# Kernel tuning notes

Measured on AMD Instinct MI355X. Metric: run time of the kernel, lower is better.

## Reference

```python
import jax, jax.numpy as jnp
import numpy as np

NPOINT = 1024
BRANCHES = [(0.4, 32), (0.8, 64)]  # (radius, nsample)
SPECS = [[67, 64, 64, 128], [67, 64, 128, 256]]  # mlp specs after use_xyz (+3)
EPS = 1e-5


def setup_inputs() -> dict:
    key = jax.random.key(0)
    ks = jax.random.split(key, 16)
    B, N, C = 8, 8192, 64
    inp = {
        "xyz": jax.random.normal(ks[0], (B, N, 3), jnp.float32),
        "features": jax.random.normal(ks[1], (B, C, N), jnp.float32),
    }
    ki = 2
    for bi, spec in enumerate(SPECS):
        for li in range(3):
            o, i = spec[li + 1], spec[li]
            inp[f"w{bi}_{li}"] = jax.random.normal(ks[ki], (o, i), jnp.float32) * (1.0 / np.sqrt(i)); ki += 1
            inp[f"g{bi}_{li}"] = jnp.ones((o,), jnp.float32)
            inp[f"b{bi}_{li}"] = jnp.zeros((o,), jnp.float32)
    return inp


def fps(pts, npoint):
    # pts: [B, N+1, 3] (mean point prepended); sequential farthest point sampling
    B, N1, _ = pts.shape

    def step(carry, _):
        dist, far = carry
        idx3 = jnp.broadcast_to(far[:, None, None], (B, 1, 3))
        centroid = jnp.take_along_axis(pts, idx3, axis=1)  # [B,1,3]
        d = jnp.sum((pts - centroid) ** 2, axis=-1)        # [B,N+1]
        dist = jnp.minimum(dist, d)
        far2 = jnp.argmax(dist, axis=-1)
        return (dist, far2), centroid[:, 0, :]

    dist0 = jnp.full((B, N1), 1e10, jnp.float32)
    far0 = jnp.zeros((B,), jnp.int32)
    _, locs = jax.lax.scan(step, (dist0, far0), None, length=npoint)
    return jnp.transpose(locs, (1, 0, 2))  # [B, npoint, 3]


def ball_query(xyz, new_xyz, radius, nsample):
    # first <=nsample indices with dist^2 < radius^2, padded with first valid (0 if none)
    B, N, _ = xyz.shape
    d2 = jnp.sum((new_xyz[:, :, None, :] - xyz[:, None, :, :]) ** 2, axis=-1)  # [B,S,N]
    score = jnp.where(d2 < radius * radius, jnp.arange(N, dtype=jnp.int32), N)
    vals, _ = jax.lax.top_k(-score, nsample)  # smallest scores = earliest valid indices
    idx = -vals                               # [B,S,nsample], N marks invalid
    first = idx[..., :1]
    first = jnp.where(first < N, first, 0)
    return jnp.where(idx < N, idx, first)


def _forward(xyz, features, params):
    mean = jnp.mean(xyz, axis=1, keepdims=True)
    pts = jnp.concatenate([mean, xyz], axis=1)          # prepend mean point
    new_xyz = jax.lax.stop_gradient(fps(pts, NPOINT))   # [B,npoint,3] (torch no_grad)
    outs = []
    for (radius, nsample), layers in zip(BRANCHES, params):
        idx = ball_query(xyz, new_xyz, radius, nsample)           # [B,S,K]
        gxyz = jax.vmap(lambda p, i: p[i])(xyz, idx)              # [B,S,K,3]
        rel = jnp.transpose(gxyz - new_xyz[:, :, None, :], (0, 3, 1, 2))  # [B,3,S,K]
        gfeat = jax.vmap(lambda f, i: f[:, i])(features, idx)     # [B,C,S,K]
        x = jnp.concatenate([rel, gfeat], axis=1)                 # [B,3+C,S,K]
        for W, g, b in layers:  # Conv2d 1x1 (no bias) + BatchNorm (train stats) + ReLU
            x = jnp.einsum('oi,bisk->bosk', W, x)
            m = jnp.mean(x, axis=(0, 2, 3), keepdims=True)
            v = jnp.var(x, axis=(0, 2, 3), keepdims=True)
            x = (x - m) / jnp.sqrt(v + EPS) * g[None, :, None, None] + b[None, :, None, None]
            x = jax.nn.relu(x)
        outs.append(jnp.max(x, axis=3))                           # [B,Cout,S]
    return new_xyz, jnp.concatenate(outs, axis=1)


def reference(xyz, features,
              w0_0, g0_0, b0_0, w0_1, g0_1, b0_1, w0_2, g0_2, b0_2,
              w1_0, g1_0, b1_0, w1_1, g1_1, b1_1, w1_2, g1_2, b1_2):
    params = [
        [(w0_0, g0_0, b0_0), (w0_1, g0_1, b0_1), (w0_2, g0_2, b0_2)],
        [(w1_0, g1_0, b1_0), (w1_1, g1_1, b1_1), (w1_2, g1_2, b1_2)],
    ]
    return _forward(xyz, features, params)
```

## Files before the change

### kernel.cpp

```cpp
#include <hip/hip_runtime.h>
#include <hip/hip_bf16.h>
#include <cstdint>


typedef __attribute__((ext_vector_type(8))) short short8;
typedef __attribute__((ext_vector_type(4))) float f32x4;
typedef __attribute__((ext_vector_type(2))) float f32x2;

__device__ __forceinline__ float bf2f(unsigned short u) {
    return __uint_as_float(((unsigned)u) << 16);
}
__device__ __forceinline__ unsigned short f2bf(float f) {
    unsigned u = __float_as_uint(f);
    return (unsigned short)((u + 0x7fffu + ((u >> 16) & 1u)) >> 16);
}

__device__ __forceinline__ float wave_red_max_f32(float v) {
#define DPPSTEP(ctrl)                                                                  \
    {                                                                                  \
        int _t = __builtin_amdgcn_update_dpp((int)0xFF800000, __float_as_int(v), ctrl, \
                                             0xf, 0xf, false);                         \
        v = fmaxf(v, __int_as_float(_t));                                              \
    }
    DPPSTEP(0x111) DPPSTEP(0x112) DPPSTEP(0x114) DPPSTEP(0x118) DPPSTEP(0x142) DPPSTEP(0x143)
#undef DPPSTEP
    return v;
}
__device__ __forceinline__ unsigned wave_red_min_u32(unsigned v) {
#define DPPSTEP(ctrl)                                                                   \
    {                                                                                   \
        unsigned _t = (unsigned)__builtin_amdgcn_update_dpp((int)0xFFFFFFFF, (int)v,    \
                                                            ctrl, 0xf, 0xf, false);     \
        v = v < _t ? v : _t;                                                            \
    }
    DPPSTEP(0x111) DPPSTEP(0x112) DPPSTEP(0x114) DPPSTEP(0x118) DPPSTEP(0x142) DPPSTEP(0x143)
#undef DPPSTEP
    return v;
}
__device__ __forceinline__ unsigned long long u64max(unsigned long long a, unsigned long long b) {
    return a > b ? a : b;
}
__device__ __forceinline__ unsigned u32min(unsigned a, unsigned b) { return a < b ? a : b; }

static const size_t OFF_WBF   = 0;
static const size_t OFF_STATS = 262144;
static const size_t STATS_BYTES = 720896;
static const size_t OFF_AFF   = 1048576;
static const size_t OFF_IDX0  = 2097152;
static const size_t OFF_IDX1  = 3145728;
static const size_t OFF_MX    = 5242880;
static const size_t OFF_MN    = 13631488;
static const size_t OFF_Y0    = 22020096;
static const size_t OFF_Y1    = 90177536;
static const size_t OFF_FEATT = 211812352;

__global__ __launch_bounds__(256) void fused_pre(
    const float* __restrict__ xyz, const float* __restrict__ feat,
    float* __restrict__ newxyz, unsigned short* __restrict__ ft,
    const float* __restrict__ w0, const float* __restrict__ w1, const float* __restrict__ w2,
    const float* __restrict__ w3, const float* __restrict__ w4, const float* __restrict__ w5,
    unsigned short* __restrict__ wb) {
    __shared__ union alignas(16) SM {
        struct {
            float ptsx[8200], ptsy[8200], ptsz[8200];
            float ldsM[16][3];
            float meanv[3];
            unsigned long long sKey[2][4];
            float cbuf[3072];
        } f;
        float tile[64][65];
    } sm;
    const int tid = threadIdx.x;

    if (blockIdx.x >= 1032) {
        int id = (int)(blockIdx.x - 1032) * 256 + tid;
        const int psz[6] = {6144, 4096, 8192, 6144, 8192, 32768};
        const int Kp[6] = {96, 64, 64, 96, 64, 128};
        const int Ks[6] = {67, 64, 64, 67, 64, 128};
        const float* wp[6] = {w0, w1, w2, w3, w4, w5};
        int off = 0;
        for (int l = 0; l < 6; ++l) {
            if (id < off + psz[l]) {
                int e = id - off;
                int m = e / Kp[l], k = e - m * Kp[l];
                float v = (k < Ks[l]) ? wp[l][m * Ks[l] + k] : 0.f;
                wb[id] = f2bf(v);
                return;
            }
            off += psz[l];
        }
        return;
    }

    if (blockIdx.x >= 8) {
        int tb = (int)blockIdx.x - 8;
        int b = tb >> 7;
        int j0 = (tb & 127) * 64;
#pragma unroll
        for (int i = 0; i < 16; ++i) {
            int e = i * 256 + tid;
            int c = e >> 6, j = e & 63;
            sm.tile[j][c] = feat[((size_t)b * 64 + c) * 8192 + j0 + j];
        }
        __syncthreads();
#pragma unroll
        for (int i = 0; i < 16; ++i) {
            int e = i * 256 + tid;
            int j = e >> 6, c = e & 63;
            ft[((size_t)(b * 8192 + j0 + j)) * 96 + 3 + c] = f2bf(sm.tile[j][c]);
        }
        if (tid < 64) {
            int j = tid;
            size_t base = ((size_t)(b * 8192 + j0 + j)) * 96;
            const float* xp = xyz + ((size_t)b * 8192 + j0 + j) * 3;
            ft[base + 0] = f2bf(xp[0]);
            ft[base + 1] = f2bf(xp[1]);
            ft[base + 2] = f2bf(xp[2]);
        } else if (tid < 128) {
            int j = tid - 64;
            size_t base = ((size_t)(b * 8192 + j0 + j)) * 96;
            for (int c = 67; c < 96; ++c) ft[base + c] = 0;
        }
        return;
    }

    const int b = blockIdx.x;
    const int t = tid;
    const int lane = t & 63, wv = t >> 6;
    const float* xb = xyz + (size_t)b * 8192 * 3;

    f32x2 px[16], py[16], pz[16], d[16];
#pragma unroll
    for (int k = 0; k < 16; ++k) {
        int q0 = t + 256 * (2 * k);
        int q1 = t + 256 * (2 * k + 1);
        px[k].x = xb[q0 * 3 + 0]; px[k].y = xb[q1 * 3 + 0];
        py[k].x = xb[q0 * 3 + 1]; py[k].y = xb[q1 * 3 + 1];
        pz[k].x = xb[q0 * 3 + 2]; pz[k].y = xb[q1 * 3 + 2];
        d[k].x = 1e10f; d[k].y = 1e10f;
        sm.f.ptsx[q0 + 1] = px[k].x; sm.f.ptsx[q1 + 1] = px[k].y;
        sm.f.ptsy[q0 + 1] = py[k].x; sm.f.ptsy[q1 + 1] = py[k].y;
        sm.f.ptsz[q0 + 1] = pz[k].x; sm.f.ptsz[q1 + 1] = pz[k].y;
    }
    {
        float sx[4], sy[4], sz[4];
#pragma unroll
        for (int m = 0; m < 4; ++m) {
            int u = (t + 256 * m + 1023) & 1023;
            float ax = 0.f, ay = 0.f, az = 0.f;
#pragma unroll
            for (int jj = 0; jj < 8; ++jj) {
                int ia = u + 1024 * jj;
                ax += xb[ia * 3 + 0]; ay += xb[ia * 3 + 1]; az += xb[ia * 3 + 2];
            }
            sx[m] = ax; sy[m] = ay; sz[m] = az;
        }
#pragma unroll
        for (int off = 32; off; off >>= 1) {
#pragma unroll
            for (int m = 0; m < 4; ++m) {
                sx[m] += __shfl_xor(sx[m], off, 64);
                sy[m] += __shfl_xor(sy[m], off, 64);
                sz[m] += __shfl_xor(sz[m], off, 64);
            }
        }
        if (lane == 0) {
#pragma unroll
            for (int m = 0; m < 4; ++m) {
                sm.f.ldsM[wv + 4 * m][0] = sx[m];
                sm.f.ldsM[wv + 4 * m][1] = sy[m];
                sm.f.ldsM[wv + 4 * m][2] = sz[m];
            }
        }
    }
    __syncthreads();
    if (t < 3) {
        float s = 0.f;
        for (int w = 0; w < 16; ++w) s += sm.f.ldsM[w][t];
        sm.f.meanv[t] = s * (1.f / 8192.f);
    }
    __syncthreads();
    float cx = sm.f.meanv[0], cy = sm.f.meanv[1], cz = sm.f.meanv[2];
    const float mmx = cx, mmy = cy, mmz = cz;
    float dm = 1e10f;
    if (t == 0) { sm.f.ptsx[0] = cx; sm.f.ptsy[0] = cy; sm.f.ptsz[0] = cz; }
    __syncthreads();

    for (int it = 0; it < 1024; ++it) {
        if (t == 0) {
            sm.f.cbuf[it * 3 + 0] = cx;
            sm.f.cbuf[it * 3 + 1] = cy;
            sm.f.cbuf[it * 3 + 2] = cz;
        }
        f32x2 c0, c1, c2, vm2;
        c0.x = cx; c0.y = cx; c1.x = cy; c1.y = cy; c2.x = cz; c2.y = cz;
        vm2.x = -1e30f; vm2.y = -1e30f;
        {
#pragma clang fp contract(off)
#pragma unroll
            for (int k = 0; k < 16; ++k) {
                f32x2 dx = px[k] - c0;
                f32x2 dy = py[k] - c1;
                f32x2 dz = pz[k] - c2;
                f32x2 dd = (dx * dx + dy * dy) + dz * dz;
                f32x2 nd = __builtin_elementwise_min(d[k], dd);
                d[k] = nd;
                vm2 = __builtin_elementwise_max(vm2, nd);
            }
        }
        float vmax = fmaxf(vm2.x, vm2.y);
        if (t == 0) {
            float dx = __fsub_rn(mmx, cx);
            float dy = __fsub_rn(mmy, cy);
            float dz = __fsub_rn(mmz, cz);
            float dd = __fadd_rn(__fadd_rn(__fmul_rn(dx, dx), __fmul_rn(dy, dy)), __fmul_rn(dz, dz));
            dm = fminf(dm, dd);
            vmax = fmaxf(vmax, dm);
        }
        float wm = wave_red_max_f32(vmax);
        float bmaxw = __int_as_float(__builtin_amdgcn_readlane(__float_as_int(wm), 63));
        unsigned m2[16];
#pragma unroll
        for (int k = 0; k < 16; ++k) {
            unsigned i0 = (d[k].x == bmaxw) ? (unsigned)(t + 256 * (2 * k) + 1) : 0xFFFFFFFFu;
            unsigned i1 = (d[k].y == bmaxw) ? (unsigned)(t + 256 * (2 * k + 1) + 1) : 0xFFFFFFFFu;
            m2[k] = u32min(i0, i1);
        }
#pragma unroll
        for (int s = 8; s; s >>= 1)
#pragma unroll
            for (int k = 0; k < s; ++k) m2[k] = u32min(m2[k], m2[k + s]);
        unsigned mi = m2[0];
        if (t == 0 && dm == bmaxw) mi = 0u;
        unsigned wmin = wave_red_min_u32(mi);
        unsigned miw = (unsigned)__builtin_amdgcn_readlane((int)wmin, 63);
        int par = it & 1;
        if (lane == 0)
            sm.f.sKey[par][wv] = ((unsigned long long)__float_as_uint(bmaxw) << 32) |
                                 (unsigned long long)(8192u - miw);
        __syncthreads();
        unsigned long long ka[4];
#pragma unroll
        for (int i = 0; i < 4; ++i) ka[i] = sm.f.sKey[par][i];
        unsigned long long kk = u64max(u64max(ka[0], ka[1]), u64max(ka[2], ka[3]));
        int far = 8192 - (int)(unsigned)(kk & 0xffffffffull);
        cx = sm.f.ptsx[far];
        cy = sm.f.ptsy[far];
        cz = sm.f.ptsz[far];
    }
    __syncthreads();
    float* ob = newxyz + (size_t)b * 3072;
#pragma unroll
    for (int i = 0; i < 12; ++i) ob[t + 256 * i] = sm.f.cbuf[t + 256 * i];
}

__global__ void ball_query2(const float* __restrict__ xyz, const float* __restrict__ newxyz,
                            int* __restrict__ idx0, int* __restrict__ idx1) {
    int bid = blockIdx.x;
    int br = (bid >= 2048);
    int K = br ? 64 : 32;
    float r2 = br ? (0.8f * 0.8f) : (0.4f * 0.4f);
    int* idxout = br ? idx1 : idx0;
    int wid = (((bid & 2047) * 256) + threadIdx.x) >> 6;
    int lane = threadIdx.x & 63;
    int b = wid >> 10;
    const float* q = newxyz + (size_t)wid * 3;
    float qx = q[0], qy = q[1], qz = q[2];
    const float* xb = xyz + (size_t)b * 8192 * 3;
    int* out = idxout + (size_t)wid * K;
    int count = 0;
    int first = 0;
    for (int base = 0; base < 8192 && count < K; base += 64) {
        int j = base + lane;
        float dx = __fsub_rn(xb[j * 3 + 0], qx);
        float dy = __fsub_rn(xb[j * 3 + 1], qy);
        float dz = __fsub_rn(xb[j * 3 + 2], qz);
        float d2 = __fadd_rn(__fadd_rn(__fmul_rn(dx, dx), __fmul_rn(dy, dy)), __fmul_rn(dz, dz));
        bool in = d2 < r2;
        unsigned long long m = __ballot(in);
        if (count == 0 && m) first = base + __ffsll((long long)m) - 1;
        if (in) {
            int pos = count + __popcll(m & ((1ull << lane) - 1ull));
            if (pos < K) out[pos] = j;
        }
        count += __popcll(m);
    }
    if (count < K) {
        int fillv = (count > 0) ? first : 0;
        for (int p = count + lane; p < K; p += 64) out[p] = fillv;
    }
}

template <int Mp, int Kp, int IN_MODE, int OUT_MODE, int KSH, int NT>
__global__ __launch_bounds__(256) void gemm_mfma(
    const unsigned short* __restrict__ Wb, const unsigned short* __restrict__ Xin,
    const float* __restrict__ aff, const int* __restrict__ idx,
    const unsigned short* __restrict__ ftp, const float* __restrict__ newxyz,
    unsigned short* __restrict__ Yout, float* __restrict__ MX, float* __restrict__ MN,
    float* __restrict__ statS, float* __restrict__ statQ) {
    constexpr int MT = Mp / 64;
    constexpr int KS = Kp / 32;
    constexpr int NC = NT * 16;
    constexpr int NCHUNK = NT * KS * 64;
    __shared__ unsigned short Bs[NCHUNK * 8];
    __shared__ float sAux[NT * 64];
    int* sAuxI = (int*)sAux;

    const int tid = threadIdx.x;
    const int w = tid >> 6;
    const int lane = tid & 63;
    const int n = lane & 15;
    const int quad = lane >> 4;
    const int rbase = w * (Mp / 4);
    const long col0 = (long)blockIdx.x * NC;

    short8 a[MT][KS];
#pragma unroll
    for (int mt = 0; mt < MT; ++mt)
#pragma unroll
        for (int ks = 0; ks < KS; ++ks)
            a[mt][ks] = *(const short8*)(Wb + (size_t)(rbase + mt * 16 + n) * Kp + ks * 32 + quad * 8);

    if constexpr (IN_MODE == 0) {
        for (int c = tid; c < NC; c += 256) {
            long colg = col0 + c;
            sAuxI[c] = idx[colg];
            long sk = colg >> KSH;
            sAux[NC + c] = newxyz[sk * 3 + 0];
            sAux[2 * NC + c] = newxyz[sk * 3 + 1];
            sAux[3 * NC + c] = newxyz[sk * 3 + 2];
        }
    } else {
        if (tid < 2 * Kp) sAux[tid] = aff[tid];
    }
    __syncthreads();

#pragma unroll
    for (int i = 0; i < NCHUNK / 256; ++i) {
        int p = i * 256 + tid;
        int pl = p & 63;
        int pn = pl & 15;
        int pq = pl >> 4;
        int rest = p >> 6;
        int pks = rest % KS;
        int pnt = rest / KS;
        int col = pnt * 16 + pn;
        int kc = pks * 4 + pq;
        short8 v;
        if constexpr (IN_MODE == 0) {
            const int bb = (int)(col0 >> (KSH + 10));
            int j = sAuxI[col];
            v = *(const short8*)(ftp + ((long)(bb * 8192 + j)) * 96 + kc * 8);
            if (kc == 0) {
                v[0] = (short)f2bf(bf2f((unsigned short)v[0]) - sAux[NC + col]);
                v[1] = (short)f2bf(bf2f((unsigned short)v[1]) - sAux[2 * NC + col]);
                v[2] = (short)f2bf(bf2f((unsigned short)v[2]) - sAux[3 * NC + col]);
            }
        } else {
            short8 raw = *(const short8*)(Xin + (col0 + col) * (long)Kp + kc * 8);
#pragma unroll
            for (int e = 0; e < 8; ++e) {
                float xf = bf2f((unsigned short)raw[e]);
                xf = fmaxf(fmaf(xf, sAux[kc * 8 + e], sAux[Kp + kc * 8 + e]), 0.f);
                v[e] = (short)f2bf(xf);
            }
        }
        *(short8*)(&Bs[p * 8]) = v;
    }
    __syncthreads();

    f32x4 acc[MT][NT];
#pragma unroll
    for (int mt = 0; mt < MT; ++mt)
#pragma unroll
        for (int nt = 0; nt < NT; ++nt)
#pragma unroll
            for (int r = 0; r < 4; ++r) acc[mt][nt][r] = 0.f;

#pragma unroll
    for (int ks = 0; ks < KS; ++ks) {
#pragma unroll
        for (int nt = 0; nt < NT; ++nt) {
            short8 bfr = *(const short8*)(&Bs[((nt * KS + ks) * 64 + lane) * 8]);
#pragma unroll
            for (int mt = 0; mt < MT; ++mt)
                acc[mt][nt] = __builtin_amdgcn_mfma_f32_16x16x32_bf16(a[mt][ks], bfr, acc[mt][nt], 0, 0, 0);
        }
    }

    const int slot = (int)(blockIdx.x & 127);
#pragma unroll
    for (int mt = 0; mt < MT; ++mt)
#pragma unroll
        for (int r = 0; r < 4; ++r) {
            float s = 0.f, q = 0.f;
#pragma unroll
            for (int nt = 0; nt < NT; ++nt) {
                float v = acc[mt][nt][r];
                s += v;
                q = fmaf(v, v, q);
            }
#pragma unroll
            for (int off = 1; off < 16; off <<= 1) {
                s += __shfl_xor(s, off, 16);
                q += __shfl_xor(q, off, 16);
            }
            if (n == 0) {
                int ch = rbase + mt * 16 + quad * 4 + r;
                atomicAdd(statS + (size_t)ch * 128 + slot, s);
                atomicAdd(statQ + (size_t)ch * 128 + slot, q);
            }
        }

    if constexpr (OUT_MODE == 0) {
#pragma unroll
        for (int mt = 0; mt < MT; ++mt)
#pragma unroll
            for (int nt = 0; nt < NT; ++nt) {
                long col = col0 + nt * 16 + n;
                unsigned p0 = f2bf(acc[mt][nt][0]) | ((unsigned)f2bf(acc[mt][nt][1]) << 16);
                unsigned p1 = f2bf(acc[mt][nt][2]) | ((unsigned)f2bf(acc[mt][nt][3]) << 16);
                uint2 st; st.x = p0; st.y = p1;
                *(uint2*)(Yout + col * Mp + rbase + mt * 16 + quad * 4) = st;
            }
    } else {
        constexpr int GRP = (1 << KSH) / 16;
        constexpr int NG = NT / GRP;
#pragma unroll
        for (int mt = 0; mt < MT; ++mt)
#pragma unroll
            for (int r = 0; r < 4; ++r) {
#pragma unroll
                for (int gh = 0; gh < NG; ++gh) {
                    float mx = acc[mt][GRP * gh][r], mn = acc[mt][GRP * gh][r];
#pragma unroll
                    for (int e = 1; e < GRP; ++e) {
                        mx = fmaxf(mx, acc[mt][GRP * gh + e][r]);
                        mn = fminf(mn, acc[mt][GRP * gh + e][r]);
                    }
#pragma unroll
                    for (int off = 1; off < 16; off <<= 1) {
                        mx = fmaxf(mx, __shfl_xor(mx, off, 16));
                        mn = fminf(mn, __shfl_xor(mn, off, 16));
                    }
                    if (n == 0) {
                        int ch = rbase + mt * 16 + quad * 4 + r;
                        long g = (col0 >> KSH) + gh;
                        MX[(long)ch * 8192 + g] = mx;
                        MN[(long)ch * 8192 + g] = mn;
                    }
                }
            }
    }
}

__global__ void finalize_kernel(const float* __restrict__ sS, const float* __restrict__ sQ,
                                const float* __restrict__ g, const float* __restrict__ b,
                                float* __restrict__ aff, int C, float invCount) {
    int c = threadIdx.x + blockIdx.x * blockDim.x;
    if (c >= C) return;
    float s = 0.f, q = 0.f;
    for (int k = 0; k < 128; ++k) { s += sS[c * 128 + k]; q += sQ[c * 128 + k]; }
    float mean = s * invCount;
    float var = fmaxf(q * invCount - mean * mean, 0.f);
    float sc = g[c] / sqrtf(var + 1e-5f);
    float sh = b[c] - mean * sc;
    aff[c] = sc;
    aff[C + c] = sh;
}

__global__ void final_out_kernel(const float* __restrict__ MX, const float* __restrict__ MN,
                                 const float* __restrict__ aff, float* __restrict__ out1,
                                 int Cout, int cOff) {
    long i = (long)blockIdx.x * 256 + threadIdx.x;
    int c = (int)(i >> 13);
    int gidx = (int)(i & 8191);
    int b = gidx >> 10, s = gidx & 1023;
    float sc = aff[c], sh = aff[Cout + c];
    float v = fmaxf(fmaxf(sc * MX[i] + sh, sc * MN[i] + sh), 0.f);
    out1[((long)b * 384 + cOff + c) * 1024 + s] = v;
}

extern "C" void kernel_launch(void* const* d_in, const int* in_sizes, int n_in,
                              void* d_out, int out_size, void* d_ws, size_t ws_size,
                              hipStream_t stream) {
    const float* xyz = (const float*)d_in[0];
    const float* feat = (const float*)d_in[1];
    const float *W[6], *G[6], *Bi[6];
    for (int l = 0; l < 6; ++l) {
        W[l] = (const float*)d_in[2 + l * 3];
        G[l] = (const float*)d_in[3 + l * 3];
        Bi[l] = (const float*)d_in[4 + l * 3];
    }
    char* ws = (char*)d_ws;
    float* out0 = (float*)d_out;
    float* out1 = (float*)d_out + 24576;

    unsigned short* wb = (unsigned short*)(ws + OFF_WBF);
    float* stats = (float*)(ws + OFF_STATS);
    float* affine = (float*)(ws + OFF_AFF);
    int* idx0 = (int*)(ws + OFF_IDX0);
    int* idx1 = (int*)(ws + OFF_IDX1);
    float* mx = (float*)(ws + OFF_MX);
    float* mn = (float*)(ws + OFF_MN);
    unsigned short* y0 = (unsigned short*)(ws + OFF_Y0);
    unsigned short* y1 = (unsigned short*)(ws + OFF_Y1);
    unsigned short* ftp = (unsigned short*)(ws + OFF_FEATT);

    hipMemsetAsync(stats, 0, STATS_BYTES, stream);
    fused_pre<<<1288, 256, 0, stream>>>(xyz, feat, out0, ftp, W[0], W[1], W[2], W[3], W[4],
                                        W[5], wb);
    ball_query2<<<4096, 256, 0, stream>>>(xyz, out0, idx0, idx1);

    const int wOff[6] = {0, 6144, 10240, 18432, 24576, 32768};
    int stOff[6], afOff[6];
    {
        const int Cs[6] = {64, 64, 128, 64, 128, 256};
        int so = 0, ao = 0;
        for (int l = 0; l < 6; ++l) {
            stOff[l] = so; so += Cs[l] * 256;
            afOff[l] = ao; ao += Cs[l] * 2;
        }
    }

    for (int br = 0; br < 2; ++br) {
        const int K = br ? 64 : 32;
        const long NCOL = 8L * 1024 * K;
        int* idx = br ? idx1 : idx0;
        const int l0 = br * 3, l1 = br * 3 + 1, l2 = br * 3 + 2;
        const int M2 = br ? 256 : 128;
        const float invCount = 1.f / (float)NCOL;
        const int nblk256 = (int)(NCOL / 256);
        const int nblk128 = (int)(NCOL / 128);
        const int nblk64 = (int)(NCOL / 64);

        if (br == 0) {
            gemm_mfma<64, 96, 0, 0, 5, 16><<<nblk256, 256, 0, stream>>>(
                wb + wOff[l0], nullptr, nullptr, idx, ftp, out0, y0, nullptr, nullptr,
                stats + stOff[l0], stats + stOff[l0] + 64 * 128);
            finalize_kernel<<<1, 256, 0, stream>>>(stats + stOff[l0], stats + stOff[l0] + 64 * 128,
                                                   G[l0], Bi[l0], affine + afOff[l0], 64, invCount);
            gemm_mfma<64, 64, 1, 0, 5, 16><<<nblk256, 256, 0, stream>>>(
                wb + wOff[l1], y0, affine + afOff[l0], nullptr, nullptr, nullptr, y1, nullptr,
                nullptr, stats + stOff[l1], stats + stOff[l1] + 64 * 128);
            finalize_kernel<<<1, 256, 0, stream>>>(stats + stOff[l1], stats + stOff[l1] + 64 * 128,
                                                   G[l1], Bi[l1], affine + afOff[l1], 64, invCount);
            gemm_mfma<128, 64, 1, 1, 5, 8><<<nblk128, 256, 0, stream>>>(
                wb + wOff[l2], y1, affine + afOff[l1], nullptr, nullptr, nullptr, nullptr, mx, mn,
                stats + stOff[l2], stats + stOff[l2] + 128 * 128);
            finalize_kernel<<<1, 256, 0, stream>>>(stats + stOff[l2], stats + stOff[l2] + 128 * 128,
                                                   G[l2], Bi[l2], affine + afOff[l2], 128, invCount);
        } else {
            gemm_mfma<64, 96, 0, 0, 6, 16><<<nblk256, 256, 0, stream>>>(
                wb + wOff[l0], nullptr, nullptr, idx, ftp, out0, y0, nullptr, nullptr,
                stats + stOff[l0], stats + stOff[l0] + 64 * 128);
            finalize_kernel<<<1, 256, 0, stream>>>(stats + stOff[l0], stats + stOff[l0] + 64 * 128,
                                                   G[l0], Bi[l0], affine + afOff[l0], 64, invCount);
            gemm_mfma<128, 64, 1, 0, 6, 8><<<nblk128, 256, 0, stream>>>(
                wb + wOff[l1], y0, affine + afOff[l0], nullptr, nullptr, nullptr, y1, nullptr,
                nullptr, stats + stOff[l1], stats + stOff[l1] + 128 * 128);
            finalize_kernel<<<1, 256, 0, stream>>>(stats + stOff[l1], stats + stOff[l1] + 128 * 128,
                                                   G[l1], Bi[l1], affine + afOff[l1], 128, invCount);
            gemm_mfma<256, 128, 1, 1, 6, 4><<<nblk64, 256, 0, stream>>>(
                wb + wOff[l2], y1, affine + afOff[l1], nullptr, nullptr, nullptr, nullptr, mx, mn,
                stats + stOff[l2], stats + stOff[l2] + 256 * 128);
            finalize_kernel<<<1, 256, 0, stream>>>(stats + stOff[l2], stats + stOff[l2] + 256 * 128,
                                                   G[l2], Bi[l2], affine + afOff[l2], 256, invCount);
        }

        final_out_kernel<<<(M2 * 8192) / 256, 256, 0, stream>>>(mx, mn, affine + afOff[l2], out1,
                                                                M2, br ? 128 : 0);
    }
}
```

Baseline: 1.635 ms.

## Add persistent double-buffered GEMM for MLP layers and single-pass FPS argmax

The FPS loop now tracks the running max value and its index in one pass, replacing the second equality scan and min-reduction tree over all distances, and reads the per-wave keys with vector loads. The later MLP GEMMs become persistent kernels with a fixed grid of 768 blocks. Each block double-buffers the next tile's normalised and activated input in shared memory while computing the current tile, and keeps BN statistics in registers before a final atomic flush. The gather-based first layer is split into its own kernel, and the second layer of branch 0 uses a narrower NT tile. The aim is to cut FPS per-iteration work and hide load latency in the GEMMs, at the cost of more register pressure and strided tile scheduling.

```diff
diff --git a/kernel.cpp b/kernel.cpp
--- a/kernel.cpp
+++ b/kernel.cpp
@@ -65,7 +65,7 @@
             float ptsx[8200], ptsy[8200], ptsz[8200];
             float ldsM[16][3];
             float meanv[3];
-            unsigned long long sKey[2][4];
+            alignas(16) unsigned long long sKey[2][4];
             float cbuf[3072];
         } f;
         float tile[64][65];
@@ -192,9 +192,10 @@
             sm.f.cbuf[it * 3 + 1] = cy;
             sm.f.cbuf[it * 3 + 2] = cz;
         }
-        f32x2 c0, c1, c2, vm2;
+        f32x2 c0, c1, c2;
         c0.x = cx; c0.y = cx; c1.x = cy; c1.y = cy; c2.x = cz; c2.y = cz;
-        vm2.x = -1e30f; vm2.y = -1e30f;
+        float bv = -1e30f;
+        unsigned bi = 0u;
         {
 #pragma clang fp contract(off)
 #pragma unroll
@@ -205,32 +206,25 @@
                 f32x2 dd = (dx * dx + dy * dy) + dz * dz;
                 f32x2 nd = __builtin_elementwise_min(d[k], dd);
                 d[k] = nd;
-                vm2 = __builtin_elementwise_max(vm2, nd);
-            }
-        }
-        float vmax = fmaxf(vm2.x, vm2.y);
+                bool g0 = nd.x > bv;
+                bv = fmaxf(bv, nd.x);
+                bi = g0 ? (unsigned)(t + 256 * (2 * k) + 1) : bi;
+                bool g1 = nd.y > bv;
+                bv = fmaxf(bv, nd.y);
+                bi = g1 ? (unsigned)(t + 256 * (2 * k + 1) + 1) : bi;
+            }
+        }
         if (t == 0) {
             float dx = __fsub_rn(mmx, cx);
             float dy = __fsub_rn(mmy, cy);
             float dz = __fsub_rn(mmz, cz);
             float dd = __fadd_rn(__fadd_rn(__fmul_rn(dx, dx), __fmul_rn(dy, dy)), __fmul_rn(dz, dz));
             dm = fminf(dm, dd);
-            vmax = fmaxf(vmax, dm);
-        }
-        float wm = wave_red_max_f32(vmax);
+            bv = fmaxf(bv, dm);
+        }
+        float wm = wave_red_max_f32(bv);
         float bmaxw = __int_as_float(__builtin_amdgcn_readlane(__float_as_int(wm), 63));
-        unsigned m2[16];
-#pragma unroll
-        for (int k = 0; k < 16; ++k) {
-            unsigned i0 = (d[k].x == bmaxw) ? (unsigned)(t + 256 * (2 * k) + 1) : 0xFFFFFFFFu;
-            unsigned i1 = (d[k].y == bmaxw) ? (unsigned)(t + 256 * (2 * k + 1) + 1) : 0xFFFFFFFFu;
-            m2[k] = u32min(i0, i1);
-        }
-#pragma unroll
-        for (int s = 8; s; s >>= 1)
-#pragma unroll
-            for (int k = 0; k < s; ++k) m2[k] = u32min(m2[k], m2[k + s]);
-        unsigned mi = m2[0];
+        unsigned mi = (bv == bmaxw) ? bi : 0xFFFFFFFFu;
         if (t == 0 && dm == bmaxw) mi = 0u;
         unsigned wmin = wave_red_min_u32(mi);
         unsigned miw = (unsigned)__builtin_amdgcn_readlane((int)wmin, 63);
@@ -239,10 +233,9 @@
             sm.f.sKey[par][wv] = ((unsigned long long)__float_as_uint(bmaxw) << 32) |
                                  (unsigned long long)(8192u - miw);
         __syncthreads();
-        unsigned long long ka[4];
-#pragma unroll
-        for (int i = 0; i < 4; ++i) ka[i] = sm.f.sKey[par][i];
-        unsigned long long kk = u64max(u64max(ka[0], ka[1]), u64max(ka[2], ka[3]));
+        ulonglong2 kp0 = *(const ulonglong2*)&sm.f.sKey[par][0];
+        ulonglong2 kp1 = *(const ulonglong2*)&sm.f.sKey[par][2];
+        unsigned long long kk = u64max(u64max(kp0.x, kp0.y), u64max(kp1.x, kp1.y));
         int far = 8192 - (int)(unsigned)(kk & 0xffffffffull);
         cx = sm.f.ptsx[far];
         cy = sm.f.ptsy[far];
@@ -291,13 +284,11 @@
     }
 }
 
-template <int Mp, int Kp, int IN_MODE, int OUT_MODE, int KSH, int NT>
-__global__ __launch_bounds__(256) void gemm_mfma(
-    const unsigned short* __restrict__ Wb, const unsigned short* __restrict__ Xin,
-    const float* __restrict__ aff, const int* __restrict__ idx,
+template <int Mp, int Kp, int KSH, int NT>
+__global__ __launch_bounds__(256) void gemm_gather(
+    const unsigned short* __restrict__ Wb, const int* __restrict__ idx,
     const unsigned short* __restrict__ ftp, const float* __restrict__ newxyz,
-    unsigned short* __restrict__ Yout, float* __restrict__ MX, float* __restrict__ MN,
-    float* __restrict__ statS, float* __restrict__ statQ) {
+    unsigned short* __restrict__ Yout, float* __restrict__ statS, float* __restrict__ statQ) {
     constexpr int MT = Mp / 64;
     constexpr int KS = Kp / 32;
     constexpr int NC = NT * 16;
@@ -321,17 +312,13 @@
         for (int ks = 0; ks < KS; ++ks)
             a[mt][ks] = *(const short8*)(Wb + (size_t)(rbase + mt * 16 + n) * Kp + ks * 32 + quad * 8);
 
-    if constexpr (IN_MODE == 0) {
-        for (int c = tid; c < NC; c += 256) {
-            long colg = col0 + c;
-            sAuxI[c] = idx[colg];
-            long sk = colg >> KSH;
-            sAux[NC + c] = newxyz[sk * 3 + 0];
-            sAux[2 * NC + c] = newxyz[sk * 3 + 1];
-            sAux[3 * NC + c] = newxyz[sk * 3 + 2];
-        }
-    } else {
-        if (tid < 2 * Kp) sAux[tid] = aff[tid];
+    for (int c = tid; c < NC; c += 256) {
+        long colg = col0 + c;
+        sAuxI[c] = idx[colg];
+        long sk = colg >> KSH;
+        sAux[NC + c] = newxyz[sk * 3 + 0];
+        sAux[2 * NC + c] = newxyz[sk * 3 + 1];
+        sAux[3 * NC + c] = newxyz[sk * 3 + 2];
     }
     __syncthreads();
 
@@ -346,24 +333,13 @@
         int pnt = rest / KS;
         int col = pnt * 16 + pn;
         int kc = pks * 4 + pq;
-        short8 v;
-        if constexpr (IN_MODE == 0) {
-            const int bb = (int)(col0 >> (KSH + 10));
-            int j = sAuxI[col];
-            v = *(const short8*)(ftp + ((long)(bb * 8192 + j)) * 96 + kc * 8);
-            if (kc == 0) {
-                v[0] = (short)f2bf(bf2f((unsigned short)v[0]) - sAux[NC + col]);
-                v[1] = (short)f2bf(bf2f((unsigned short)v[1]) - sAux[2 * NC + col]);
-                v[2] = (short)f2bf(bf2f((unsigned short)v[2]) - sAux[3 * NC + col]);
-            }
-        } else {
-            short8 raw = *(const short8*)(Xin + (col0 + col) * (long)Kp + kc * 8);
-#pragma unroll
-            for (int e = 0; e < 8; ++e) {
-                float xf = bf2f((unsigned short)raw[e]);
-                xf = fmaxf(fmaf(xf, sAux[kc * 8 + e], sAux[Kp + kc * 8 + e]), 0.f);
-                v[e] = (short)f2bf(xf);
-            }
+        const int bb = (int)(col0 >> (KSH + 10));
+        int j = sAuxI[col];
+        short8 v = *(const short8*)(ftp + ((long)(bb * 8192 + j)) * 96 + kc * 8);
+        if (kc == 0) {
+            v[0] = (short)f2bf(bf2f((unsigned short)v[0]) - sAux[NC + col]);
+            v[1] = (short)f2bf(bf2f((unsigned short)v[1]) - sAux[2 * NC + col]);
+            v[2] = (short)f2bf(bf2f((unsigned short)v[2]) - sAux[3 * NC + col]);
         }
         *(short8*)(&Bs[p * 8]) = v;
     }
@@ -412,46 +388,191 @@
             }
         }
 
-    if constexpr (OUT_MODE == 0) {
+#pragma unroll
+    for (int mt = 0; mt < MT; ++mt)
+#pragma unroll
+        for (int nt = 0; nt < NT; ++nt) {
+            long col = col0 + nt * 16 + n;
+            unsigned p0 = f2bf(acc[mt][nt][0]) | ((unsigned)f2bf(acc[mt][nt][1]) << 16);
+            unsigned p1 = f2bf(acc[mt][nt][2]) | ((unsigned)f2bf(acc[mt][nt][3]) << 16);
+            uint2 st; st.x = p0; st.y = p1;
+            *(uint2*)(Yout + col * Mp + rbase + mt * 16 + quad * 4) = st;
+        }
+}
+
+#define STAGE_IN1(TILE, BUFI)                                                       \
+    {                                                                               \
+        long scol0 = (long)(TILE) * NC;                                             \
+        short8 raw[CPT];                                                            \
+        _Pragma("unroll") for (int i = 0; i < CPT; ++i)                             \
+            raw[i] = *(const short8*)(Xin + (scol0 + colC[i]) * (long)Kp + kcC[i] * 8); \
+        _Pragma("unroll") for (int i = 0; i < CPT; ++i) {                           \
+            short8 v;                                                               \
+            _Pragma("unroll") for (int e = 0; e < 8; ++e) {                         \
+                float xf = bf2f((unsigned short)raw[i][e]);                         \
+                xf = fmaxf(fmaf(xf, sAff[kcC[i] * 8 + e], sAff[Kp + kcC[i] * 8 + e]), 0.f); \
+                v[e] = (short)f2bf(xf);                                             \
+            }                                                                       \
+            *(short8*)(&Bs[(BUFI)][(i * 256 + tid) * 8]) = v;                       \
+        }                                                                           \
+    }
+
+template <int Mp, int Kp, int OUT_MODE, int KSH, int NT>
+__global__ __launch_bounds__(256) void gemm_pers(
+    const unsigned short* __restrict__ Wb, const unsigned short* __restrict__ Xin,
+    const float* __restrict__ aff, unsigned short* __restrict__ Yout,
+    float* __restrict__ MX, float* __restrict__ MN,
+    float* __restrict__ statS, float* __restrict__ statQ, int ntiles) {
+    constexpr int MT = Mp / 64;
+    constexpr int KS = Kp / 32;
+    constexpr int NC = NT * 16;
+    constexpr int NCHUNK = NT * KS * 64;
+    constexpr int CPT = NCHUNK / 256;
+    __shared__ unsigned short Bs[2][NCHUNK * 8];
+    __shared__ float sAff[2 * 128];
+
+    const int tid = threadIdx.x;
+    const int w = tid >> 6;
+    const int lane = tid & 63;
+    const int n = lane & 15;
+    const int quad = lane >> 4;
+    const int rbase = w * (Mp / 4);
+
+    int colC[CPT], kcC[CPT];
+    {
+        int pl = tid & 63;
+        int pn = pl & 15;
+        int pq = pl >> 4;
+#pragma unroll
+        for (int i = 0; i < CPT; ++i) {
+            int rest = i * 4 + (tid >> 6);
+            int pks = rest % KS;
+            int pnt = rest / KS;
+            colC[i] = pnt * 16 + pn;
+            kcC[i] = pks * 4 + pq;
+        }
+    }
+
+    short8 a[MT][KS];
+#pragma unroll
+    for (int mt = 0; mt < MT; ++mt)
+#pragma unroll
+        for (int ks = 0; ks < KS; ++ks)
+            a[mt][ks] = *(const short8*)(Wb + (size_t)(rbase + mt * 16 + n) * Kp + ks * 32 + quad * 8);
+
+    if (tid < 2 * Kp) sAff[tid] = aff[tid];
+    float accS[MT][4], accQ[MT][4];
+#pragma unroll
+    for (int mt = 0; mt < MT; ++mt)
+#pragma unroll
+        for (int r = 0; r < 4; ++r) { accS[mt][r] = 0.f; accQ[mt][r] = 0.f; }
+    __syncthreads();
+
+    if ((int)blockIdx.x < ntiles) STAGE_IN1((int)blockIdx.x, 0);
+    __syncthreads();
+
+    int g = 0;
+    for (int t = (int)blockIdx.x; t < ntiles; t += (int)gridDim.x, ++g) {
+        int tn = t + (int)gridDim.x;
+        if (tn < ntiles) STAGE_IN1(tn, (g + 1) & 1);
+
+        const int cur = g & 1;
+        const long col0 = (long)t * NC;
+        f32x4 acc[MT][NT];
 #pragma unroll
         for (int mt = 0; mt < MT; ++mt)
 #pragma unroll
+            for (int nt = 0; nt < NT; ++nt)
+#pragma unroll
+                for (int r = 0; r < 4; ++r) acc[mt][nt][r] = 0.f;
+
+#pragma unroll
+        for (int ks = 0; ks < KS; ++ks) {
+#pragma unroll
             for (int nt = 0; nt < NT; ++nt) {
-                long col = col0 + nt * 16 + n;
-                unsigned p0 = f2bf(acc[mt][nt][0]) | ((unsigned)f2bf(acc[mt][nt][1]) << 16);
-                unsigned p1 = f2bf(acc[mt][nt][2]) | ((unsigned)f2bf(acc[mt][nt][3]) << 16);
-                uint2 st; st.x = p0; st.y = p1;
-                *(uint2*)(Yout + col * Mp + rbase + mt * 16 + quad * 4) = st;
-            }
-    } else {
-        constexpr int GRP = (1 << KSH) / 16;
-        constexpr int NG = NT / GRP;
+                short8 bfr = *(const short8*)(&Bs[cur][((nt * KS + ks) * 64 + lane) * 8]);
+#pragma unroll
+                for (int mt = 0; mt < MT; ++mt)
+                    acc[mt][nt] =
+                        __builtin_amdgcn_mfma_f32_16x16x32_bf16(a[mt][ks], bfr, acc[mt][nt], 0, 0, 0);
+            }
+        }
+
 #pragma unroll
         for (int mt = 0; mt < MT; ++mt)
 #pragma unroll
             for (int r = 0; r < 4; ++r) {
-#pragma unroll
-                for (int gh = 0; gh < NG; ++gh) {
-                    float mx = acc[mt][GRP * gh][r], mn = acc[mt][GRP * gh][r];
-#pragma unroll
-                    for (int e = 1; e < GRP; ++e) {
-                        mx = fmaxf(mx, acc[mt][GRP * gh + e][r]);
-                        mn = fminf(mn, acc[mt][GRP * gh + e][r]);
-                    }
-#pragma unroll
-                    for (int off = 1; off < 16; off <<= 1) {
-                        mx = fmaxf(mx, __shfl_xor(mx, off, 16));
-                        mn = fminf(mn, __shfl_xor(mn, off, 16));
-                    }
-                    if (n == 0) {
-                        int ch = rbase + mt * 16 + quad * 4 + r;
-                        long g = (col0 >> KSH) + gh;
-                        MX[(long)ch * 8192 + g] = mx;
-                        MN[(long)ch * 8192 + g] = mn;
+                float s = accS[mt][r], q = accQ[mt][r];
+#pragma unroll
+                for (int nt = 0; nt < NT; ++nt) {
+                    float v = acc[mt][nt][r];
+                    s += v;
+                    q = fmaf(v, v, q);
+                }
+                accS[mt][r] = s;
+                accQ[mt][r] = q;
+            }
+
+        if constexpr (OUT_MODE == 0) {
+#pragma unroll
+            for (int mt = 0; mt < MT; ++mt)
+#pragma unroll
+                for (int nt = 0; nt < NT; ++nt) {
+                    long col = col0 + nt * 16 + n;
+                    unsigned p0 = f2bf(acc[mt][nt][0]) | ((unsigned)f2bf(acc[mt][nt][1]) << 16);
+                    unsigned p1 = f2bf(acc[mt][nt][2]) | ((unsigned)f2bf(acc[mt][nt][3]) << 16);
+                    uint2 st; st.x = p0; st.y = p1;
+                    *(uint2*)(Yout + col * Mp + rbase + mt * 16 + quad * 4) = st;
+                }
+        } else {
+            constexpr int GRP = (1 << KSH) / 16;
+            constexpr int NG = NT / GRP;
+#pragma unroll
+            for (int mt = 0; mt < MT; ++mt)
+#pragma unroll
+                for (int r = 0; r < 4; ++r) {
+#pragma unroll
+                    for (int gh = 0; gh < NG; ++gh) {
+                        float mx = acc[mt][GRP * gh][r], mn = acc[mt][GRP * gh][r];
+#pragma unroll
+                        for (int e = 1; e < GRP; ++e) {
+                            mx = fmaxf(mx, acc[mt][GRP * gh + e][r]);
+                            mn = fminf(mn, acc[mt][GRP * gh + e][r]);
+                        }
+#pragma unroll
+                        for (int off = 1; off < 16; off <<= 1) {
+                            mx = fmaxf(mx, __shfl_xor(mx, off, 16));
+                            mn = fminf(mn, __shfl_xor(mn, off, 16));
+                        }
+                        if (n == 0) {
+                            int ch = rbase + mt * 16 + quad * 4 + r;
+                            long gg = (col0 >> KSH) + gh;
+                            MX[(long)ch * 8192 + gg] = mx;
+                            MN[(long)ch * 8192 + gg] = mn;
+                        }
                     }
                 }
-            }
-    }
+        }
+        __syncthreads();
+    }
+
+    const int slot = (int)(blockIdx.x & 127);
+#pragma unroll
+    for (int mt = 0; mt < MT; ++mt)
+#pragma unroll
+        for (int r = 0; r < 4; ++r) {
+            float s = accS[mt][r], q = accQ[mt][r];
+#pragma unroll
+            for (int off = 1; off < 16; off <<= 1) {
+                s += __shfl_xor(s, off, 16);
+                q += __shfl_xor(q, off, 16);
+            }
+            if (n == 0) {
+                int ch = rbase + mt * 16 + quad * 4 + r;
+                atomicAdd(statS + (size_t)ch * 128 + slot, s);
+                atomicAdd(statQ + (size_t)ch * 128 + slot, q);
+            }
+        }
 }
 
 __global__ void finalize_kernel(const float* __restrict__ sS, const float* __restrict__ sQ,
@@ -522,53 +643,41 @@
             afOff[l] = ao; ao += Cs[l] * 2;
         }
     }
-
-    for (int br = 0; br < 2; ++br) {
-        const int K = br ? 64 : 32;
-        const long NCOL = 8L * 1024 * K;
-        int* idx = br ? idx1 : idx0;
-        const int l0 = br * 3, l1 = br * 3 + 1, l2 = br * 3 + 2;
-        const int M2 = br ? 256 : 128;
-        const float invCount = 1.f / (float)NCOL;
-        const int nblk256 = (int)(NCOL / 256);
-        const int nblk128 = (int)(NCOL / 128);
-        const int nblk64 = (int)(NCOL / 64);
-
-        if (br == 0) {
-            gemm_mfma<64, 96, 0, 0, 5, 16><<<nblk256, 256, 0, stream>>>(
-                wb + wOff[l0], nullptr, nullptr, idx, ftp, out0, y0, nullptr, nullptr,
-                stats + stOff[l0], stats + stOff[l0] + 64 * 128);
-            finalize_kernel<<<1, 256, 0, stream>>>(stats + stOff[l0], stats + stOff[l0] + 64 * 128,
-                                                   G[l0], Bi[l0], affine + afOff[l0], 64, invCount);
-            gemm_mfma<64, 64, 1, 0, 5, 16><<<nblk256, 256, 0, stream>>>(
-                wb + wOff[l1], y0, affine + afOff[l0], nullptr, nullptr, nullptr, y1, nullptr,
-                nullptr, stats + stOff[l1], stats + stOff[l1] + 64 * 128);
-            finalize_kernel<<<1, 256, 0, stream>>>(stats + stOff[l1], stats + stOff[l1] + 64 * 128,
-                                                   G[l1], Bi[l1], affine + afOff[l1], 64, invCount);
-            gemm_mfma<128, 64, 1, 1, 5, 8><<<nblk128, 256, 0, stream>>>(
-                wb + wOff[l2], y1, affine + afOff[l1], nullptr, nullptr, nullptr, nullptr, mx, mn,
-                stats + stOff[l2], stats + stOff[l2] + 128 * 128);
-            finalize_kernel<<<1, 256, 0, stream>>>(stats + stOff[l2], stats + stOff[l2] + 128 * 128,
-                                                   G[l2], Bi[l2], affine + afOff[l2], 128, invCount);
-        } else {
-            gemm_mfma<64, 96, 0, 0, 6, 16><<<nblk256, 256, 0, stream>>>(
-                wb + wOff[l0], nullptr, nullptr, idx, ftp, out0, y0, nullptr, nullptr,
-                stats + stOff[l0], stats + stOff[l0] + 64 * 128);
-            finalize_kernel<<<1, 256, 0, stream>>>(stats + stOff[l0], stats + stOff[l0] + 64 * 128,
-                                                   G[l0], Bi[l0], affine + afOff[l0], 64, invCount);
-            gemm_mfma<128, 64, 1, 0, 6, 8><<<nblk128, 256, 0, stream>>>(
-                wb + wOff[l1], y0, affine + afOff[l0], nullptr, nullptr, nullptr, y1, nullptr,
-                nullptr, stats + stOff[l1], stats + stOff[l1] + 128 * 128);
-            finalize_kernel<<<1, 256, 0, stream>>>(stats + stOff[l1], stats + stOff[l1] + 128 * 128,
-                                                   G[l1], Bi[l1], affine + afOff[l1], 128, invCount);
-            gemm_mfma<256, 128, 1, 1, 6, 4><<<nblk64, 256, 0, stream>>>(
-                wb + wOff[l2], y1, affine + afOff[l1], nullptr, nullptr, nullptr, nullptr, mx, mn,
-                stats + stOff[l2], stats + stOff[l2] + 256 * 128);
-            finalize_kernel<<<1, 256, 0, stream>>>(stats + stOff[l2], stats + stOff[l2] + 256 * 128,
-                                                   G[l2], Bi[l2], affine + afOff[l2], 256, invCount);
-        }
-
-        final_out_kernel<<<(M2 * 8192) / 256, 256, 0, stream>>>(mx, mn, affine + afOff[l2], out1,
-                                                                M2, br ? 128 : 0);
-    }
-}
+    const float ic0 = 1.f / (float)(8L * 1024 * 32);
+    const float ic1 = 1.f / (float)(8L * 1024 * 64);
+    const int GRID = 768;
+
+    gemm_gather<64, 96, 5, 16><<<1024, 256, 0, stream>>>(
+        wb + wOff[0], idx0, ftp, out0, y0, stats + stOff[0], stats + stOff[0] + 64 * 128);
+    finalize_kernel<<<1, 256, 0, stream>>>(stats + stOff[0], stats + stOff[0] + 64 * 128,
+                                           G[0], Bi[0], affine + afOff[0], 64, ic0);
+    gemm_pers<64, 64, 0, 5, 8><<<GRID, 256, 0, stream>>>(
+        wb + wOff[1], y0, affine + afOff[0], y1, nullptr, nullptr, stats + stOff[1],
+        stats + stOff[1] + 64 * 128, 2048);
+    finalize_kernel<<<1, 256, 0, stream>>>(stats + stOff[1], stats + stOff[1] + 64 * 128,
+                                           G[1], Bi[1], affine + afOff[1], 64, ic0);
+    gemm_pers<128, 64, 1, 5, 8><<<GRID, 256, 0, stream>>>(
+        wb + wOff[2], y1, affine + afOff[1], nullptr, mx, mn, stats + stOff[2],
+        stats + stOff[2] + 128 * 128, 2048);
+    finalize_kernel<<<1, 256, 0, stream>>>(stats + stOff[2], stats + stOff[2] + 128 * 128,
+                                           G[2], Bi[2], affine + afOff[2], 128, ic0);
+    final_out_kernel<<<(128 * 8192) / 256, 256, 0, stream>>>(mx, mn, affine + afOff[2], out1,
+                                                             128, 0);
+
+    gemm_gather<64, 96, 6, 16><<<2048, 256, 0, stream>>>(
+        wb + wOff[3], idx1, ftp, out0, y0, stats + stOff[3], stats + stOff[3] + 64 * 128);
+    finalize_kernel<<<1, 256, 0, stream>>>(stats + stOff[3], stats + stOff[3] + 64 * 128,
+                                           G[3], Bi[3], affine + afOff[3], 64, ic1);
+    gemm_pers<128, 64, 0, 6, 8><<<GRID, 256, 0, stream>>>(
+        wb + wOff[4], y0, affine + afOff[3], y1, nullptr, nullptr, stats + stOff[4],
+        stats + stOff[4] + 128 * 128, 4096);
+    finalize_kernel<<<1, 256, 0, stream>>>(stats + stOff[4], stats + stOff[4] + 128 * 128,
+                                           G[4], Bi[4], affine + afOff[4], 128, ic1);
+    gemm_pers<256, 128, 1, 6, 4><<<GRID, 256, 0, stream>>>(
+        wb + wOff[5], y1, affine + afOff[4], nullptr, mx, mn, stats + stOff[5],
+        stats + stOff[5] + 256 * 128, 8192);
+    finalize_kernel<<<1, 256, 0, stream>>>(stats + stOff[5], stats + stOff[5] + 256 * 128,
+                                           G[5], Bi[5], affine + afOff[5], 256, ic1);
+    final_out_kernel<<<(256 * 8192) / 256, 256, 0, stream>>>(mx, mn, affine + afOff[5], out1,
+                                                             256, 128);
+}
```

Result: faster. 1.523 ms (-6.9%).
